# Performance work log

Hardware: AMD Instinct MI355X
Metric: run time of the kernel (lower is better)

## Reference

```python
import jax, jax.numpy as jnp
import numpy as np

K = 3
DILATION = 1
DG = 1  # deformable groups


def _deform_conv2d(x, offsets, mask, weight, bias, k=K, dilation=DILATION, dg=DG):
    # x: [B, C, H, W]; offsets: [B, dg*2*k*k, H, W]; mask: [B, dg*k*k, H, W]
    # weight: [O, C, k, k]; bias: [O]
    B, C, H, W = x.shape
    O = weight.shape[0]
    Cg = C // dg
    kk = k * k
    pad = (k // 2) * dilation

    # base sampling grid per kernel tap (stride=1)
    ky, kx = jnp.meshgrid(jnp.arange(k), jnp.arange(k), indexing='ij')
    ky = ky.reshape(kk)
    kx = kx.reshape(kk)
    base_y = (jnp.arange(H)[None, :, None] - pad + ky[:, None, None] * dilation)  # [kk,H,1]
    base_x = (jnp.arange(W)[None, None, :] - pad + kx[:, None, None] * dilation)  # [kk,1,W]

    off = offsets.reshape(B, dg, kk, 2, H, W)
    py = base_y[None, None].astype(x.dtype) + off[:, :, :, 0]  # [B,dg,kk,H,W]
    px = base_x[None, None].astype(x.dtype) + off[:, :, :, 1]  # [B,dg,kk,H,W]

    y0 = jnp.floor(py)
    x0 = jnp.floor(px)
    wy1 = py - y0  # frac weights
    wx1 = px - x0
    wy0 = 1.0 - wy1
    wx0 = 1.0 - wx1

    img = x.reshape(B, dg, Cg, H * W)

    def gather(yi, xi):
        # yi, xi: float integer-valued coords [B,dg,kk,H,W]; zero outside bounds
        valid = (yi >= 0) & (yi <= H - 1) & (xi >= 0) & (xi <= W - 1)
        yc = jnp.clip(yi, 0, H - 1).astype(jnp.int32)
        xc = jnp.clip(xi, 0, W - 1).astype(jnp.int32)
        idx = (yc * W + xc).reshape(B, dg, 1, kk * H * W)
        vals = jnp.take_along_axis(img, idx, axis=3).reshape(B, dg, Cg, kk, H, W)
        return vals * valid.reshape(B, dg, 1, kk, H, W).astype(x.dtype)

    def w5(a):  # lift [B,dg,kk,H,W] -> [B,dg,1,kk,H,W]
        return a.reshape(B, dg, 1, kk, H, W)

    sampled = (gather(y0, x0) * w5(wy0 * wx0)
               + gather(y0, x0 + 1) * w5(wy0 * wx1)
               + gather(y0 + 1, x0) * w5(wy1 * wx0)
               + gather(y0 + 1, x0 + 1) * w5(wy1 * wx1))  # [B,dg,Cg,kk,H,W]

    sampled = sampled * mask.reshape(B, dg, 1, kk, H, W)
    sampled = sampled.reshape(B, C, kk, H, W)

    out = jnp.einsum('bckhw,ock->bohw', sampled, weight.reshape(O, C, kk))
    return out + bias[None, :, None, None]


def setup_inputs() -> dict:
    key = jax.random.key(0)
    k1, k2, k3, k4, k5 = jax.random.split(key, 5)
    B, C, O, H, W = 8, 128, 128, 64, 64
    x = jax.random.normal(k1, (B, C, H, W), dtype=jnp.float32)
    offsets = jax.random.normal(k2, (B, DG * 2 * K * K, H, W), dtype=jnp.float32)
    mask = jax.random.uniform(k3, (B, DG * K * K, H, W), dtype=jnp.float32)
    fan_in = C * K * K
    weight = jax.random.normal(k4, (O, C, K, K), dtype=jnp.float32) / np.sqrt(fan_in)
    bias = jax.random.normal(k5, (O,), dtype=jnp.float32) * 0.01
    return {"x": x, "offsets": offsets, "mask": mask, "weight": weight, "bias": bias}


def reference(x, offsets, mask, weight, bias):
    return _deform_conv2d(x, offsets, mask, weight, bias)
```

## Files before the change

### kernel.cpp

```cpp
#include <hip/hip_runtime.h>
#include <math.h>

constexpr int Bn = 8, Cn = 128, On = 128, Hn = 64, Wn = 64;
constexpr int KK = 9, PAD = 1;
constexpr int BDIM = 512;
constexpr int PXB  = 64;
constexpr int CG = 16, NG = Cn / CG;
constexpr int KG = 160, KTOT = NG * KG;
constexpr int BANDH = 11;
constexpr int XSTP = 716;
constexpr int AST  = 81;
constexpr int ME   = KK * PXB;
constexpr int PB_DW  = 8 * XSTP;
constexpr int ASH_DW = PXB * AST;
constexpr int SM_DW  = PB_DW + 2 * ASH_DW;
constexpr int BUNITS = BANDH * 128;

typedef __attribute__((ext_vector_type(8))) short bf16x8;
typedef __attribute__((ext_vector_type(4))) float f32x4;
typedef unsigned short u16;
typedef unsigned int u32;

__device__ __forceinline__ u16 f2bf(float f) {
    union { float f; u32 u; } v; v.f = f;
    return (u16)((v.u + 0x7FFFu + ((v.u >> 16) & 1u)) >> 16);
}
__device__ __forceinline__ u32 cpk(float a, float b) {
    u32 r;
    asm("v_cvt_pk_bf16_f32 %0, %1, %2" : "=v"(r) : "v"(a), "v"(b));
    return r;
}
__device__ __forceinline__ float bflo(u32 w) { return __uint_as_float(w << 16); }
__device__ __forceinline__ float bfhi(u32 w) { return __uint_as_float(w & 0xFFFF0000u); }

__global__ void wprep_kernel(const float* __restrict__ w, u16* __restrict__ wbf) {
    __shared__ u32 tmpw[KTOT / 2];
    u16* tmp = (u16*)tmpw;
    const int tid = threadIdx.x, o = blockIdx.x;
    if (tid < 64)
        tmpw[(tid >> 3) * 80 + 72 + (tid & 7)] = 0;
    for (int k = tid; k < Cn * KK; k += 256) {
        const int c = k / 9, t = k - 9 * c;
        tmp[(c >> 4) * KG + t * 16 + (c & 15)] = f2bf(w[o * (Cn * KK) + k]);
    }
    __syncthreads();
    u32* dst = (u32*)(wbf + (size_t)o * KTOT);
    for (int e = tid; e < KTOT / 2; e += 256) dst[e] = tmpw[e];
}

__device__ __forceinline__ void do_sample(const u32* __restrict__ pband,
                                          u32* __restrict__ ashW,
                                          const float* __restrict__ xg,
                                          const float4 w, const int2 q,
                                          const int2 ix, const int e)
{
    const int t = e >> 6, px = e & 63;
    u32 avp[8];
    if (!__any((q.x | q.y) < 0)) {
        const u32* p0 = pband + ix.x;
        const u32* p1 = pband + ix.y;
        #pragma unroll
        for (int c2 = 0; c2 < 8; ++c2) {
            const u32 wt0 = p0[c2 * XSTP], wt1 = p0[c2 * XSTP + 1];
            const u32 wb0 = p1[c2 * XSTP], wb1 = p1[c2 * XSTP + 1];
            const float va = fmaf(w.x, bflo(wt0), fmaf(w.y, bflo(wt1),
                             fmaf(w.z, bflo(wb0), w.w * bflo(wb1))));
            const float vb = fmaf(w.x, bfhi(wt0), fmaf(w.y, bfhi(wt1),
                             fmaf(w.z, bfhi(wb0), w.w * bfhi(wb1))));
            avp[c2] = cpk(va, vb);
        }
    } else {
        const int qx = q.x < 0 ? ~q.x : q.x;
        const int qy = q.y < 0 ? ~q.y : q.y;
        const int yrx = qx >> 8, yry = qy >> 8;
        const int xx = (qx & 255) - 1, xy = (qy & 255) - 1;
        const int ax0 = max(xx, 0), ax1 = min(xx + 1, Wn - 1);
        const int ay0 = max(xy, 0), ay1 = min(xy + 1, Wn - 1);
        #pragma unroll
        for (int c2 = 0; c2 < 8; ++c2) {
            float v2[2];
            #pragma unroll
            for (int sb = 0; sb < 2; ++sb) {
                const float* gc = xg + ((2 * c2 + sb) << 12);
                const float t0 = gc[yrx * Wn + ax0], t1 = gc[yrx * Wn + ax1];
                const float b0 = gc[yry * Wn + ay0], b1 = gc[yry * Wn + ay1];
                v2[sb] = fmaf(w.x, t0, fmaf(w.y, t1, fmaf(w.z, b0, w.w * b1)));
            }
            avp[c2] = cpk(v2[0], v2[1]);
        }
    }
    u32* d = ashW + px * AST + t * 8;
    #pragma unroll
    for (int j = 0; j < 8; ++j) d[j] = avp[j];
}

__global__ __launch_bounds__(BDIM, 4)
void dcn_mfma_kernel(const float* __restrict__ x,
                     const float* __restrict__ offs,
                     const float* __restrict__ mask,
                     const u16*   __restrict__ wbf,
                     const float* __restrict__ bias,
                     float* __restrict__ out)
{
    __shared__ __align__(16) u32 smem[SM_DW];
    u32* const pband = smem;

    const int tid = threadIdx.x;
    const int b   = blockIdx.x & 7;
    const int h   = blockIdx.x >> 3;
    const int r0  = min(max(h - 5, 0), Hn - BANDH);

    const int s_px4 = tid & 15, s_pair = (tid >> 4) & 7;

    float4 bnda[3], bndb[3];
#define BLOAD(GCH) { \
        _Pragma("unroll") \
        for (int it = 0; it < 3; ++it) { \
            const int u = tid + it * BDIM; \
            if (u < BUNITS) { \
                const int row = u >> 7; \
                const float* bp = x + (((size_t)(b * Cn + (GCH) * CG + 2 * s_pair)) << 12) \
                                  + (r0 + row) * Wn + (s_px4 << 2); \
                bnda[it] = *(const float4*)bp; \
                bndb[it] = *(const float4*)(bp + 4096); \
            } \
        } }
#define BWRITE() { \
        _Pragma("unroll") \
        for (int it = 0; it < 3; ++it) { \
            const int u = tid + it * BDIM; \
            if (u < BUNITS) { \
                const int row = u >> 7; \
                u32* d = &pband[s_pair * XSTP + row * 64 + 8 + (s_px4 << 2)]; \
                *(uint4*)d = make_uint4( \
                    cpk(bnda[it].x, bndb[it].x), cpk(bnda[it].y, bndb[it].y), \
                    cpk(bnda[it].z, bndb[it].z), cpk(bnda[it].w, bndb[it].w)); \
            } \
        } }

    BLOAD(0);

    float4 mw[2]; int2 mq[2]; int2 mi[2];
    #pragma unroll
    for (int it = 0; it < 2; ++it) {
        mw[it] = make_float4(0.f, 0.f, 0.f, 0.f);
        mq[it] = make_int2(r0 << 8, r0 << 8);
        mi[it] = make_int2(7, 7);
        const int e = tid + it * BDIM;
        if (e < ME) {
            const int t = e >> 6, px = e & 63;
            const int ty = t / 3, tx = t - ty * 3;
            const float oy = offs[((b * 18 + 2 * t    ) * Hn + h) * Wn + px];
            const float ox = offs[((b * 18 + 2 * t + 1) * Hn + h) * Wn + px];
            const float m  = mask[((b * KK + t) * Hn + h) * Wn + px];
            const float py = (float)(h - PAD + ty) + oy;
            const float qx = (float)(px - PAD + tx) + ox;
            const float fy = floorf(py), fx = floorf(qx);
            const float wy1 = py - fy, wx1 = qx - fx;
            const float wy0 = 1.f - wy1, wx0 = 1.f - wx1;
            const int y0 = (int)fy, x0 = (int)fx;
            const bool cx0 = (x0 >= 0) && (x0 < Wn);
            const bool cx1 = (x0 >= -1) && (x0 < Wn - 1);
            const float wr[2] = { wy0, wy1 };
            float wout[4]; int qout[2], iout[2];
            #pragma unroll
            for (int j = 0; j < 2; ++j) {
                const int yr = y0 + j;
                const bool rv = (yr >= 0) && (yr < Hn);
                wout[2 * j]     = (rv && cx0) ? wr[j] * wx0 * m : 0.f;
                wout[2 * j + 1] = (rv && cx1) ? wr[j] * wx1 * m : 0.f;
                int qv;
                if (!rv || (!cx0 && !cx1)) qv = r0 << 8;
                else                       qv = (yr << 8) | (x0 + 1);
                const bool inband = (qv >> 8) >= r0 && (qv >> 8) < r0 + BANDH;
                qout[j] = inband ? qv : ~qv;
                iout[j] = (((qv >> 8) - r0) << 6) + (qv & 255) + 7;
            }
            mw[it] = make_float4(wout[0], wout[1], wout[2], wout[3]);
            mq[it] = make_int2(qout[0], qout[1]);
            mi[it] = make_int2(iout[0], iout[1]);
        }
    }

    if (tid < 128) {
        const int pr = tid >> 4, ws = tid & 15;
        if (ws < 12) pband[pr * XSTP + (ws < 8 ? ws : 704 + ws)] = 0;
    }
    #pragma unroll
    for (int it = 0; it < 2; ++it) {
        const int u = tid + it * BDIM;
        smem[PB_DW + (u >> 9) * ASH_DW + ((u & 511) >> 3) * AST + 72 + (u & 7)] = 0;
    }

    BWRITE();
    BLOAD(1);
    __syncthreads();

    const int wv = tid >> 6, ln = tid & 63, quad = ln >> 4, l16 = ln & 15;
    const int mrow = wv >> 1, ncol = wv & 1;
    const u16* wrow0 = wbf + (size_t)(mrow * 32 + l16) * KTOT;
    const int npx0 = ncol * 32 + l16, npx1 = npx0 + 16;

    {
        const float* xg = x + (((size_t)(b * Cn)) << 12);
        do_sample(pband, smem + PB_DW, xg, mw[0], mq[0], mi[0], tid);
        if (tid < 64)
            do_sample(pband, smem + PB_DW, xg, mw[1], mq[1], mi[1], BDIM + tid);
    }
    __syncthreads();

    f32x4 acc[2][2];
    #pragma unroll
    for (int mt = 0; mt < 2; ++mt)
        #pragma unroll
        for (int nt = 0; nt < 2; ++nt) acc[mt][nt] = (f32x4){0.f, 0.f, 0.f, 0.f};

    bf16x8 pa0[2], pa1[2];
#define APRE(GG) { const int kgp = (GG) * KG + quad * 8; \
        pa0[0] = *(const bf16x8*)(wrow0 + kgp); \
        pa1[0] = *(const bf16x8*)(wrow0 + 16 * KTOT + kgp); \
        pa0[1] = *(const bf16x8*)(wrow0 + kgp + 32); \
        pa1[1] = *(const bf16x8*)(wrow0 + 16 * KTOT + kgp + 32); }
    APRE(0);

#define MSTEP_PRE(S) { \
        union BF { bf16x8 v; u32 w[4]; } b0, b1; \
        const int kd = (S) * 16 + quad * 4; \
        _Pragma("unroll") \
        for (int j = 0; j < 4; ++j) { \
            b0.w[j] = ad[npx0 * AST + kd + j]; \
            b1.w[j] = ad[npx1 * AST + kd + j]; \
        } \
        acc[0][0] = __builtin_amdgcn_mfma_f32_16x16x32_bf16(pa0[S], b0.v, acc[0][0], 0, 0, 0); \
        acc[0][1] = __builtin_amdgcn_mfma_f32_16x16x32_bf16(pa0[S], b1.v, acc[0][1], 0, 0, 0); \
        acc[1][0] = __builtin_amdgcn_mfma_f32_16x16x32_bf16(pa1[S], b0.v, acc[1][0], 0, 0, 0); \
        acc[1][1] = __builtin_amdgcn_mfma_f32_16x16x32_bf16(pa1[S], b1.v, acc[1][1], 0, 0, 0); }

#define MSTEP_LD(S) { \
        const int kg = g * KG + (S) * 32 + quad * 8; \
        const bf16x8 a0 = *(const bf16x8*)(wrow0 + kg); \
        const bf16x8 a1 = *(const bf16x8*)(wrow0 + 16 * KTOT + kg); \
        union BF { bf16x8 v; u32 w[4]; } b0, b1; \
        const int kd = (S) * 16 + quad * 4; \
        _Pragma("unroll") \
        for (int j = 0; j < 4; ++j) { \
            b0.w[j] = ad[npx0 * AST + kd + j]; \
            b1.w[j] = ad[npx1 * AST + kd + j]; \
        } \
        acc[0][0] = __builtin_amdgcn_mfma_f32_16x16x32_bf16(a0, b0.v, acc[0][0], 0, 0, 0); \
        acc[0][1] = __builtin_amdgcn_mfma_f32_16x16x32_bf16(a0, b1.v, acc[0][1], 0, 0, 0); \
        acc[1][0] = __builtin_amdgcn_mfma_f32_16x16x32_bf16(a1, b0.v, acc[1][0], 0, 0, 0); \
        acc[1][1] = __builtin_amdgcn_mfma_f32_16x16x32_bf16(a1, b1.v, acc[1][1], 0, 0, 0); }

    for (int g = 0; g < NG; ++g) {
        const u32* ad = smem + PB_DW + (g & 1) * ASH_DW;
        u32* ashN     = smem + PB_DW + ((g + 1) & 1) * ASH_DW;
        if (g + 1 < NG) BWRITE();
        MSTEP_PRE(0);
        MSTEP_PRE(1);
        __syncthreads();
        if (g + 2 < NG) BLOAD(g + 2);
        if (g + 1 < NG) {
            const float* xg = x + (((size_t)(b * Cn + (g + 1) * CG)) << 12);
            do_sample(pband, ashN, xg, mw[0], mq[0], mi[0], tid);
            if (tid < 64)
                do_sample(pband, ashN, xg, mw[1], mq[1], mi[1], BDIM + tid);
        }
        MSTEP_LD(2);
        MSTEP_LD(3);
        MSTEP_LD(4);
        if (g + 1 < NG) APRE(g + 1);
        __syncthreads();
    }

    float* tr = (float*)smem;
    #pragma unroll
    for (int mt = 0; mt < 2; ++mt)
        #pragma unroll
        for (int nt = 0; nt < 2; ++nt)
            #pragma unroll
            for (int r = 0; r < 4; ++r) {
                const int o  = mrow * 32 + mt * 16 + quad * 4 + r;
                const int px = ncol * 32 + nt * 16 + l16;
                tr[o * 68 + px] = acc[mt][nt][r] + bias[o];
            }
    __syncthreads();
    {
        const int orow = tid >> 2, f0 = tid & 3;
        #pragma unroll
        for (int it = 0; it < 4; ++it) {
            const int f = f0 + it * 4;
            const float4 v = *(const float4*)&tr[orow * 68 + (f << 2)];
            *(float4*)&out[(((size_t)b * On + orow) * Hn + h) * Wn + (f << 2)] = v;
        }
    }
#undef BLOAD
#undef BWRITE
#undef APRE
#undef MSTEP_PRE
#undef MSTEP_LD
}

constexpr int FBD = 256;
constexpr int FB_PXB = 32, FB_CCH = 4, FB_NCT = FB_CCH * KK, FB_MW = KK * FB_PXB;

#define FMA4(A, S, W)                          \
    A.x = fmaf((S).x, (W), A.x);               \
    A.y = fmaf((S).y, (W), A.y);               \
    A.z = fmaf((S).z, (W), A.z);               \
    A.w = fmaf((S).w, (W), A.w);

__global__ __launch_bounds__(FBD, 4)
void dcn_fb_kernel(const float* __restrict__ x,
                   const float* __restrict__ offs,
                   const float* __restrict__ mask,
                   const float* __restrict__ weight,
                   const float* __restrict__ bias,
                   float* __restrict__ out)
{
    __shared__ float wmeta[4 * FB_MW];
    __shared__ int   imeta[4 * FB_MW];
    __shared__ float ssh[FB_NCT * FB_PXB];
    __shared__ float wsh[FB_NCT * On];

    const int tid    = threadIdx.x;
    const int b      = blockIdx.x & 7;
    const int rem    = blockIdx.x >> 3;
    const int h      = rem >> 1;
    const int pxbase = (rem & 1) * FB_PXB;

    for (int e = tid; e < FB_MW; e += FBD) {
        const int t  = e >> 5;
        const int px = e & 31;
        const int pg = pxbase + px;
        const int ty = t / 3, tx = t - ty * 3;
        const float oy = offs[((b * 18 + 2 * t    ) * Hn + h) * Wn + pg];
        const float ox = offs[((b * 18 + 2 * t + 1) * Hn + h) * Wn + pg];
        const float m  = mask[((b * KK + t) * Hn + h) * Wn + pg];
        const float py = (float)(h - PAD + ty) + oy;
        const float qx = (float)(pg - PAD + tx) + ox;
        const float y0 = floorf(py), x0 = floorf(qx);
        const float wy1 = py - y0, wx1 = qx - x0;
        const float wy0 = 1.f - wy1, wx0 = 1.f - wx1;
        const float cw[4] = { wy0 * wx0, wy0 * wx1, wy1 * wx0, wy1 * wx1 };
        #pragma unroll
        for (int k = 0; k < 4; ++k) {
            const float yk = y0 + (float)(k >> 1);
            const float xk = x0 + (float)(k & 1);
            const bool valid = (yk >= 0.f) && (yk <= (float)(Hn - 1)) &&
                               (xk >= 0.f) && (xk <= (float)(Wn - 1));
            const int yc = (int)fminf(fmaxf(yk, 0.f), (float)(Hn - 1));
            const int xc = (int)fminf(fmaxf(xk, 0.f), (float)(Wn - 1));
            wmeta[k * FB_MW + e] = valid ? cw[k] * m : 0.f;
            imeta[k * FB_MW + e] = yc * Wn + xc;
        }
    }
    __syncthreads();

    const int px0 = (tid & 7) << 2;
    const int oo  = (tid >> 3) << 2;

    float4 acc[4];
    #pragma unroll
    for (int j = 0; j < 4; ++j) acc[j] = make_float4(0.f, 0.f, 0.f, 0.f);

    for (int cb = 0; cb < Cn / FB_CCH; ++cb) {
        #pragma unroll
        for (int it = 0; it < (FB_NCT * On) / FBD; ++it) {
            const int e = tid + it * FBD;
            const int r = e >> 7;
            const int o = e & 127;
            wsh[r * On + o] = weight[o * (Cn * KK) + cb * FB_NCT + r];
        }
        for (int e = tid; e < FB_NCT * FB_PXB; e += FBD) {
            const int px = e & 31;
            const int ct = e >> 5;
            const int c  = ct / 9;
            const int mb = (ct - c * 9) * FB_PXB + px;
            const float* xp = x + (((b * Cn) + cb * FB_CCH + c) << 12);
            float v =  wmeta[mb]              * xp[imeta[mb]];
            v = fmaf(wmeta[FB_MW     + mb], xp[imeta[FB_MW     + mb]], v);
            v = fmaf(wmeta[2 * FB_MW + mb], xp[imeta[2 * FB_MW + mb]], v);
            v = fmaf(wmeta[3 * FB_MW + mb], xp[imeta[3 * FB_MW + mb]], v);
            ssh[ct * FB_PXB + px] = v;
        }
        __syncthreads();

        #pragma unroll 6
        for (int ct = 0; ct < FB_NCT; ++ct) {
            const float4 sv = *(const float4*)&ssh[ct * FB_PXB + px0];
            const float4 wa = *(const float4*)&wsh[ct * On + oo];
            FMA4(acc[0], sv, wa.x);
            FMA4(acc[1], sv, wa.y);
            FMA4(acc[2], sv, wa.z);
            FMA4(acc[3], sv, wa.w);
        }
        __syncthreads();
    }

    #pragma unroll
    for (int j = 0; j < 4; ++j) {
        const float bv = bias[oo + j];
        float4 r = acc[j];
        r.x += bv; r.y += bv; r.z += bv; r.w += bv;
        *(float4*)&out[((b * On + oo + j) * Hn + h) * Wn + pxbase + px0] = r;
    }
}

extern "C" void kernel_launch(void* const* d_in, const int* in_sizes, int n_in,
                              void* d_out, int out_size, void* d_ws, size_t ws_size,
                              hipStream_t stream) {
    const float* x      = (const float*)d_in[0];
    const float* offs   = (const float*)d_in[1];
    const float* mask   = (const float*)d_in[2];
    const float* weight = (const float*)d_in[3];
    const float* bias   = (const float*)d_in[4];
    float* out = (float*)d_out;

    const size_t need = (size_t)On * KTOT * sizeof(u16);
    if (d_ws != nullptr && ws_size >= need) {
        u16* wbf = (u16*)d_ws;
        wprep_kernel<<<dim3(On), dim3(256), 0, stream>>>(weight, wbf);
        dcn_mfma_kernel<<<dim3(Bn * Hn), dim3(BDIM), 0, stream>>>(
            x, offs, mask, wbf, bias, out);
    } else {
        dcn_fb_kernel<<<dim3(Bn * Hn * 2), dim3(FBD), 0, stream>>>(
            x, offs, mask, weight, bias, out);
    }
}
```

Baseline: 139.3 us.

## Switch to fp16 packed bilinear sampling and f16 MFMA with padded LDS

Converts the input band, sampling weights and conv weights from bf16 to fp16 so bilinear interpolation runs as packed half2 math instead of unpacking to fp32 FMAs. The GEMM switches to f16 MFMA, prefetches all five A-fragments per group into registers, and reads B operands with 128-bit LDS loads. Band and A-tile strides are padded (row stride 68, XSTP 756, AST 84) to allow vector stores and reduce bank conflicts. Doing the interpolation in half precision adds fp16 rounding and range risk in exchange for fewer ALU ops and higher register pressure.

```diff
diff --git a/kernel.cpp b/kernel.cpp
--- a/kernel.cpp
+++ b/kernel.cpp
@@ -8,32 +8,35 @@
 constexpr int CG = 16, NG = Cn / CG;
 constexpr int KG = 160, KTOT = NG * KG;
 constexpr int BANDH = 11;
-constexpr int XSTP = 716;
-constexpr int AST  = 81;
+constexpr int RST  = 68;
+constexpr int XSTP = 756;
+constexpr int AST  = 84;
 constexpr int ME   = KK * PXB;
 constexpr int PB_DW  = 8 * XSTP;
 constexpr int ASH_DW = PXB * AST;
 constexpr int SM_DW  = PB_DW + 2 * ASH_DW;
 constexpr int BUNITS = BANDH * 128;
 
-typedef __attribute__((ext_vector_type(8))) short bf16x8;
+typedef __attribute__((ext_vector_type(2))) _Float16 h2;
+typedef __attribute__((ext_vector_type(8))) __fp16   f16x8;
 typedef __attribute__((ext_vector_type(4))) float f32x4;
 typedef unsigned short u16;
 typedef unsigned int u32;
 
-__device__ __forceinline__ u16 f2bf(float f) {
-    union { float f; u32 u; } v; v.f = f;
-    return (u16)((v.u + 0x7FFFu + ((v.u >> 16) & 1u)) >> 16);
-}
-__device__ __forceinline__ u32 cpk(float a, float b) {
-    u32 r;
-    asm("v_cvt_pk_bf16_f32 %0, %1, %2" : "=v"(r) : "v"(a), "v"(b));
-    return r;
-}
-__device__ __forceinline__ float bflo(u32 w) { return __uint_as_float(w << 16); }
-__device__ __forceinline__ float bfhi(u32 w) { return __uint_as_float(w & 0xFFFF0000u); }
-
-__global__ void wprep_kernel(const float* __restrict__ w, u16* __restrict__ wbf) {
+union UH  { u32 u; h2 h; };
+union U4H { uint4 u; f16x8 h; };
+
+__device__ __forceinline__ u32 pkh(float a, float b) {
+    union { decltype(__builtin_amdgcn_cvt_pkrtz(0.f, 0.f)) p; u32 u; } t;
+    t.p = __builtin_amdgcn_cvt_pkrtz(a, b);
+    return t.u;
+}
+__device__ __forceinline__ h2 bch(u32 w) { UH t; t.u = w; return t.h; }
+__device__ __forceinline__ u16 f2h(float f) {
+    union { _Float16 h; u16 u; } v; v.h = (_Float16)f; return v.u;
+}
+
+__global__ void wprep_kernel(const float* __restrict__ w, u16* __restrict__ wh) {
     __shared__ u32 tmpw[KTOT / 2];
     u16* tmp = (u16*)tmpw;
     const int tid = threadIdx.x, o = blockIdx.x;
@@ -41,17 +44,17 @@
         tmpw[(tid >> 3) * 80 + 72 + (tid & 7)] = 0;
     for (int k = tid; k < Cn * KK; k += 256) {
         const int c = k / 9, t = k - 9 * c;
-        tmp[(c >> 4) * KG + t * 16 + (c & 15)] = f2bf(w[o * (Cn * KK) + k]);
+        tmp[(c >> 4) * KG + t * 16 + (c & 15)] = f2h(w[o * (Cn * KK) + k]);
     }
     __syncthreads();
-    u32* dst = (u32*)(wbf + (size_t)o * KTOT);
+    u32* dst = (u32*)(wh + (size_t)o * KTOT);
     for (int e = tid; e < KTOT / 2; e += 256) dst[e] = tmpw[e];
 }
 
 __device__ __forceinline__ void do_sample(const u32* __restrict__ pband,
                                           u32* __restrict__ ashW,
                                           const float* __restrict__ xg,
-                                          const float4 w, const int2 q,
+                                          const uint4 wp, const int2 q,
                                           const int2 ix, const int e)
 {
     const int t = e >> 6, px = e & 63;
@@ -59,17 +62,17 @@
     if (!__any((q.x | q.y) < 0)) {
         const u32* p0 = pband + ix.x;
         const u32* p1 = pband + ix.y;
+        const h2 w0 = bch(wp.x), w1 = bch(wp.y), w2 = bch(wp.z), w3 = bch(wp.w);
         #pragma unroll
         for (int c2 = 0; c2 < 8; ++c2) {
-            const u32 wt0 = p0[c2 * XSTP], wt1 = p0[c2 * XSTP + 1];
-            const u32 wb0 = p1[c2 * XSTP], wb1 = p1[c2 * XSTP + 1];
-            const float va = fmaf(w.x, bflo(wt0), fmaf(w.y, bflo(wt1),
-                             fmaf(w.z, bflo(wb0), w.w * bflo(wb1))));
-            const float vb = fmaf(w.x, bfhi(wt0), fmaf(w.y, bfhi(wt1),
-                             fmaf(w.z, bfhi(wb0), w.w * bfhi(wb1))));
-            avp[c2] = cpk(va, vb);
+            const h2 vt0 = bch(p0[c2 * XSTP]), vt1 = bch(p0[c2 * XSTP + 1]);
+            const h2 vb0 = bch(p1[c2 * XSTP]), vb1 = bch(p1[c2 * XSTP + 1]);
+            const h2 r = w0 * vt0 + w1 * vt1 + w2 * vb0 + w3 * vb1;
+            UH o; o.h = r; avp[c2] = o.u;
         }
     } else {
+        const float fw0 = (float)bch(wp.x)[0], fw1 = (float)bch(wp.y)[0];
+        const float fw2 = (float)bch(wp.z)[0], fw3 = (float)bch(wp.w)[0];
         const int qx = q.x < 0 ? ~q.x : q.x;
         const int qy = q.y < 0 ? ~q.y : q.y;
         const int yrx = qx >> 8, yry = qy >> 8;
@@ -84,21 +87,21 @@
                 const float* gc = xg + ((2 * c2 + sb) << 12);
                 const float t0 = gc[yrx * Wn + ax0], t1 = gc[yrx * Wn + ax1];
                 const float b0 = gc[yry * Wn + ay0], b1 = gc[yry * Wn + ay1];
-                v2[sb] = fmaf(w.x, t0, fmaf(w.y, t1, fmaf(w.z, b0, w.w * b1)));
+                v2[sb] = fmaf(fw0, t0, fmaf(fw1, t1, fmaf(fw2, b0, fw3 * b1)));
             }
-            avp[c2] = cpk(v2[0], v2[1]);
+            avp[c2] = pkh(v2[0], v2[1]);
         }
     }
     u32* d = ashW + px * AST + t * 8;
-    #pragma unroll
-    for (int j = 0; j < 8; ++j) d[j] = avp[j];
+    *(uint4*)&d[0] = make_uint4(avp[0], avp[1], avp[2], avp[3]);
+    *(uint4*)&d[4] = make_uint4(avp[4], avp[5], avp[6], avp[7]);
 }
 
 __global__ __launch_bounds__(BDIM, 4)
 void dcn_mfma_kernel(const float* __restrict__ x,
                      const float* __restrict__ offs,
                      const float* __restrict__ mask,
-                     const u16*   __restrict__ wbf,
+                     const u16*   __restrict__ wh,
                      const float* __restrict__ bias,
                      float* __restrict__ out)
 {
@@ -131,19 +134,19 @@
             const int u = tid + it * BDIM; \
             if (u < BUNITS) { \
                 const int row = u >> 7; \
-                u32* d = &pband[s_pair * XSTP + row * 64 + 8 + (s_px4 << 2)]; \
+                u32* d = &pband[s_pair * XSTP + row * RST + 8 + (s_px4 << 2)]; \
                 *(uint4*)d = make_uint4( \
-                    cpk(bnda[it].x, bndb[it].x), cpk(bnda[it].y, bndb[it].y), \
-                    cpk(bnda[it].z, bndb[it].z), cpk(bnda[it].w, bndb[it].w)); \
+                    pkh(bnda[it].x, bndb[it].x), pkh(bnda[it].y, bndb[it].y), \
+                    pkh(bnda[it].z, bndb[it].z), pkh(bnda[it].w, bndb[it].w)); \
             } \
         } }
 
     BLOAD(0);
 
-    float4 mw[2]; int2 mq[2]; int2 mi[2];
+    uint4 mwp[2]; int2 mq[2]; int2 mi[2];
     #pragma unroll
     for (int it = 0; it < 2; ++it) {
-        mw[it] = make_float4(0.f, 0.f, 0.f, 0.f);
+        mwp[it] = make_uint4(0, 0, 0, 0);
         mq[it] = make_int2(r0 << 8, r0 << 8);
         mi[it] = make_int2(7, 7);
         const int e = tid + it * BDIM;
@@ -174,17 +177,19 @@
                 else                       qv = (yr << 8) | (x0 + 1);
                 const bool inband = (qv >> 8) >= r0 && (qv >> 8) < r0 + BANDH;
                 qout[j] = inband ? qv : ~qv;
-                iout[j] = (((qv >> 8) - r0) << 6) + (qv & 255) + 7;
+                iout[j] = ((qv >> 8) - r0) * RST + (qv & 255) + 7;
             }
-            mw[it] = make_float4(wout[0], wout[1], wout[2], wout[3]);
+            mwp[it] = make_uint4(pkh(wout[0], wout[0]), pkh(wout[1], wout[1]),
+                                 pkh(wout[2], wout[2]), pkh(wout[3], wout[3]));
             mq[it] = make_int2(qout[0], qout[1]);
             mi[it] = make_int2(iout[0], iout[1]);
         }
     }
 
-    if (tid < 128) {
-        const int pr = tid >> 4, ws = tid & 15;
-        if (ws < 12) pband[pr * XSTP + (ws < 8 ? ws : 704 + ws)] = 0;
+    if (tid < 416) {
+        const int pair = tid / 52, j = tid - pair * 52;
+        const int off = (j < 8) ? j : RST * ((j - 8) >> 2) + 72 + ((j - 8) & 3);
+        pband[pair * XSTP + off] = 0;
     }
     #pragma unroll
     for (int it = 0; it < 2; ++it) {
@@ -198,14 +203,14 @@
 
     const int wv = tid >> 6, ln = tid & 63, quad = ln >> 4, l16 = ln & 15;
     const int mrow = wv >> 1, ncol = wv & 1;
-    const u16* wrow0 = wbf + (size_t)(mrow * 32 + l16) * KTOT;
+    const u16* wrow0 = wh + (size_t)(mrow * 32 + l16) * KTOT;
     const int npx0 = ncol * 32 + l16, npx1 = npx0 + 16;
 
     {
         const float* xg = x + (((size_t)(b * Cn)) << 12);
-        do_sample(pband, smem + PB_DW, xg, mw[0], mq[0], mi[0], tid);
+        do_sample(pband, smem + PB_DW, xg, mwp[0], mq[0], mi[0], tid);
         if (tid < 64)
-            do_sample(pband, smem + PB_DW, xg, mw[1], mq[1], mi[1], BDIM + tid);
+            do_sample(pband, smem + PB_DW, xg, mwp[1], mq[1], mi[1], BDIM + tid);
     }
     __syncthreads();
 
@@ -215,60 +220,42 @@
         #pragma unroll
         for (int nt = 0; nt < 2; ++nt) acc[mt][nt] = (f32x4){0.f, 0.f, 0.f, 0.f};
 
-    bf16x8 pa0[2], pa1[2];
+    f16x8 pa[5][2];
 #define APRE(GG) { const int kgp = (GG) * KG + quad * 8; \
-        pa0[0] = *(const bf16x8*)(wrow0 + kgp); \
-        pa1[0] = *(const bf16x8*)(wrow0 + 16 * KTOT + kgp); \
-        pa0[1] = *(const bf16x8*)(wrow0 + kgp + 32); \
-        pa1[1] = *(const bf16x8*)(wrow0 + 16 * KTOT + kgp + 32); }
+        _Pragma("unroll") \
+        for (int s = 0; s < 5; ++s) { \
+            pa[s][0] = *(const f16x8*)(wrow0 + kgp + s * 32); \
+            pa[s][1] = *(const f16x8*)(wrow0 + 16 * KTOT + kgp + s * 32); \
+        } }
     APRE(0);
 
-#define MSTEP_PRE(S) { \
-        union BF { bf16x8 v; u32 w[4]; } b0, b1; \
+#define MSTEP(S) { \
         const int kd = (S) * 16 + quad * 4; \
-        _Pragma("unroll") \
-        for (int j = 0; j < 4; ++j) { \
-            b0.w[j] = ad[npx0 * AST + kd + j]; \
-            b1.w[j] = ad[npx1 * AST + kd + j]; \
-        } \
-        acc[0][0] = __builtin_amdgcn_mfma_f32_16x16x32_bf16(pa0[S], b0.v, acc[0][0], 0, 0, 0); \
-        acc[0][1] = __builtin_amdgcn_mfma_f32_16x16x32_bf16(pa0[S], b1.v, acc[0][1], 0, 0, 0); \
-        acc[1][0] = __builtin_amdgcn_mfma_f32_16x16x32_bf16(pa1[S], b0.v, acc[1][0], 0, 0, 0); \
-        acc[1][1] = __builtin_amdgcn_mfma_f32_16x16x32_bf16(pa1[S], b1.v, acc[1][1], 0, 0, 0); }
-
-#define MSTEP_LD(S) { \
-        const int kg = g * KG + (S) * 32 + quad * 8; \
-        const bf16x8 a0 = *(const bf16x8*)(wrow0 + kg); \
-        const bf16x8 a1 = *(const bf16x8*)(wrow0 + 16 * KTOT + kg); \
-        union BF { bf16x8 v; u32 w[4]; } b0, b1; \
-        const int kd = (S) * 16 + quad * 4; \
-        _Pragma("unroll") \
-        for (int j = 0; j < 4; ++j) { \
-            b0.w[j] = ad[npx0 * AST + kd + j]; \
-            b1.w[j] = ad[npx1 * AST + kd + j]; \
-        } \
-        acc[0][0] = __builtin_amdgcn_mfma_f32_16x16x32_bf16(a0, b0.v, acc[0][0], 0, 0, 0); \
-        acc[0][1] = __builtin_amdgcn_mfma_f32_16x16x32_bf16(a0, b1.v, acc[0][1], 0, 0, 0); \
-        acc[1][0] = __builtin_amdgcn_mfma_f32_16x16x32_bf16(a1, b0.v, acc[1][0], 0, 0, 0); \
-        acc[1][1] = __builtin_amdgcn_mfma_f32_16x16x32_bf16(a1, b1.v, acc[1][1], 0, 0, 0); }
+        U4H b0, b1; \
+        b0.u = *(const uint4*)&ad[npx0 * AST + kd]; \
+        b1.u = *(const uint4*)&ad[npx1 * AST + kd]; \
+        acc[0][0] = __builtin_amdgcn_mfma_f32_16x16x32_f16(pa[S][0], b0.h, acc[0][0], 0, 0, 0); \
+        acc[0][1] = __builtin_amdgcn_mfma_f32_16x16x32_f16(pa[S][0], b1.h, acc[0][1], 0, 0, 0); \
+        acc[1][0] = __builtin_amdgcn_mfma_f32_16x16x32_f16(pa[S][1], b0.h, acc[1][0], 0, 0, 0); \
+        acc[1][1] = __builtin_amdgcn_mfma_f32_16x16x32_f16(pa[S][1], b1.h, acc[1][1], 0, 0, 0); }
 
     for (int g = 0; g < NG; ++g) {
         const u32* ad = smem + PB_DW + (g & 1) * ASH_DW;
         u32* ashN     = smem + PB_DW + ((g + 1) & 1) * ASH_DW;
         if (g + 1 < NG) BWRITE();
-        MSTEP_PRE(0);
-        MSTEP_PRE(1);
+        MSTEP(0);
+        MSTEP(1);
         __syncthreads();
         if (g + 2 < NG) BLOAD(g + 2);
         if (g + 1 < NG) {
             const float* xg = x + (((size_t)(b * Cn + (g + 1) * CG)) << 12);
-            do_sample(pband, ashN, xg, mw[0], mq[0], mi[0], tid);
+            do_sample(pband, ashN, xg, mwp[0], mq[0], mi[0], tid);
             if (tid < 64)
-                do_sample(pband, ashN, xg, mw[1], mq[1], mi[1], BDIM + tid);
-        }
-        MSTEP_LD(2);
-        MSTEP_LD(3);
-        MSTEP_LD(4);
+                do_sample(pband, ashN, xg, mwp[1], mq[1], mi[1], BDIM + tid);
+        }
+        MSTEP(2);
+        MSTEP(3);
+        MSTEP(4);
         if (g + 1 < NG) APRE(g + 1);
         __syncthreads();
     }
@@ -297,8 +284,7 @@
 #undef BLOAD
 #undef BWRITE
 #undef APRE
-#undef MSTEP_PRE
-#undef MSTEP_LD
+#undef MSTEP
 }
 
 constexpr int FBD = 256;
@@ -419,10 +405,10 @@
 
     const size_t need = (size_t)On * KTOT * sizeof(u16);
     if (d_ws != nullptr && ws_size >= need) {
-        u16* wbf = (u16*)d_ws;
-        wprep_kernel<<<dim3(On), dim3(256), 0, stream>>>(weight, wbf);
+        u16* wh = (u16*)d_ws;
+        wprep_kernel<<<dim3(On), dim3(256), 0, stream>>>(weight, wh);
         dcn_mfma_kernel<<<dim3(Bn * Hn), dim3(BDIM), 0, stream>>>(
-            x, offs, mask, wbf, bias, out);
+            x, offs, mask, wh, bias, out);
     } else {
         dcn_fb_kernel<<<dim3(Bn * Hn * 2), dim3(FBD), 0, stream>>>(
             x, offs, mask, weight, bias, out);
```

New measurement: 149.9 us. 7.7% more time.
